# Kernel optimization log

Measured on AMD Instinct MI355X. Metric: run time of the kernel, lower is better.

## Reference

```python
import jax, jax.numpy as jnp
import numpy as np

B, S, D, H, F = 2, 2048, 1024, 16, 4096
DH = D // H


def setup_inputs() -> dict:
    key = jax.random.key(0)
    ks = jax.random.split(key, 8)
    scale = 0.02
    def nrm(k, shape):
        return jax.random.normal(k, shape, jnp.float32) * scale
    return {
        "x": jax.random.normal(ks[0], (B, S, D), jnp.float32),
        "ln1_g": jnp.ones((D,), jnp.float32),
        "ln1_b": jnp.zeros((D,), jnp.float32),
        "wq": nrm(ks[1], (D, D)), "bq": jnp.zeros((D,), jnp.float32),
        "wk": nrm(ks[2], (D, D)), "bk": jnp.zeros((D,), jnp.float32),
        "wv": nrm(ks[3], (D, D)), "bv": jnp.zeros((D,), jnp.float32),
        "wo": nrm(ks[4], (D, D)), "bo": jnp.zeros((D,), jnp.float32),
        "ln2_g": jnp.ones((D,), jnp.float32),
        "ln2_b": jnp.zeros((D,), jnp.float32),
        "w1": nrm(ks[5], (D, F)), "b1": jnp.zeros((F,), jnp.float32),
        "w2": nrm(ks[6], (F, D)), "b2": jnp.zeros((D,), jnp.float32),
    }


def _layernorm(x, g, b, eps=1e-5):
    m = jnp.mean(x, axis=-1, keepdims=True)
    v = jnp.var(x, axis=-1, keepdims=True)
    return (x - m) / jnp.sqrt(v + eps) * g + b


def reference(x, ln1_g, ln1_b, wq, bq, wk, bk, wv, bv, wo, bo,
              ln2_g, ln2_b, w1, b1, w2, b2):
    # GPT2Block forward, prefill path (state=None): K/V = ln_1(x), causal mask.
    Bx, Sx, Dx = x.shape
    h = _layernorm(x, ln1_g, ln1_b)

    def heads(t):  # [B,S,D] -> [B,H,S,DH]
        return t.reshape(Bx, Sx, H, DH).transpose(0, 2, 1, 3)

    q = heads(h @ wq + bq)
    k = heads(h @ wk + bk)
    v = heads(h @ wv + bv)

    scores = jnp.einsum('bhqd,bhkd->bhqk', q, k) / jnp.sqrt(jnp.float32(DH))
    # masked_softmax: key position < valid_len (= query_pos+1) kept; else -1e6
    causal = jnp.arange(Sx)[None, :] <= jnp.arange(Sx)[:, None]  # [S,S]
    scores = jnp.where(causal, scores, jnp.float32(-1e6))
    attn_w = jax.nn.softmax(scores, axis=-1)

    o = jnp.einsum('bhqk,bhkd->bhqd', attn_w, v)
    o = o.transpose(0, 2, 1, 3).reshape(Bx, Sx, Dx)
    attn_out = o @ wo + bo

    add1 = x + attn_out  # dropout inactive (eval)
    h2 = _layernorm(add1, ln2_g, ln2_b)
    mlp = jax.nn.gelu(h2 @ w1 + b1, approximate=False) @ w2 + b2
    return add1 + mlp
```

## Files before the change

### kernel.cpp

```cpp
#include <hip/hip_runtime.h>
#include <hip/hip_bf16.h>


#define BDIM 1024
#define SEQ 2048
#define NH 16
#define DHEAD 64
#define FDIM 4096
#define QKVD 3072

typedef __attribute__((ext_vector_type(8))) short short8v;
typedef __attribute__((ext_vector_type(4))) float floatx4;

__device__ __forceinline__ unsigned short f2bf(float f) {
    unsigned int u = __float_as_uint(f);
    unsigned int r = u + 0x7FFFu + ((u >> 16) & 1u);
    return (unsigned short)(r >> 16);
}
__device__ __forceinline__ unsigned int pack2bf(float a, float b) {
    return (unsigned int)f2bf(a) | ((unsigned int)f2bf(b) << 16);
}

__device__ __forceinline__ void load16_lds(const unsigned short* g, short* l) {
    __builtin_amdgcn_global_load_lds((const __attribute__((address_space(1))) void*)g,
                                     (__attribute__((address_space(3))) void*)l, 16, 0, 0);
}

__global__ __launch_bounds__(256) void transpose_all(const float* __restrict__ wq,
                                                     const float* __restrict__ wk,
                                                     const float* __restrict__ wv,
                                                     const float* __restrict__ wo,
                                                     const float* __restrict__ w1,
                                                     const float* __restrict__ w2,
                                                     unsigned short* __restrict__ qkvT,
                                                     unsigned short* __restrict__ woT,
                                                     unsigned short* __restrict__ w1T,
                                                     unsigned short* __restrict__ w2T) {
    const int g = blockIdx.x;
    const float* W;
    unsigned short* Wt;
    int K, N, tx, ty;
    if (g < 4096) {
        const int w = g >> 10, tile = g & 1023;
        tx = tile & 31; ty = tile >> 5; K = 1024; N = 1024;
        W = (w == 0) ? wq : (w == 1) ? wk : (w == 2) ? wv : wo;
        Wt = (w == 3) ? woT : qkvT + (size_t)w * 1024 * 1024;
    } else if (g < 8192) {
        const int tile = g - 4096;
        tx = tile & 127; ty = tile >> 7; K = 1024; N = 4096;
        W = w1; Wt = w1T;
    } else {
        const int tile = g - 8192;
        tx = tile & 31; ty = tile >> 5; K = 4096; N = 1024;
        W = w2; Wt = w2T;
    }
    __shared__ float tile[32][33];
    const int t = threadIdx.x;
    const int r = t >> 3, c4 = (t & 7) * 4;
    const int n0 = tx * 32, k0 = ty * 32;
    float4 p = *(const float4*)(W + (size_t)(k0 + r) * N + n0 + c4);
    tile[r][c4 + 0] = p.x;
    tile[r][c4 + 1] = p.y;
    tile[r][c4 + 2] = p.z;
    tile[r][c4 + 3] = p.w;
    __syncthreads();
    ushort4 ou;
    ou.x = f2bf(tile[c4 + 0][r]);
    ou.y = f2bf(tile[c4 + 1][r]);
    ou.z = f2bf(tile[c4 + 2][r]);
    ou.w = f2bf(tile[c4 + 3][r]);
    *(ushort4*)(Wt + (size_t)(n0 + r) * K + k0 + c4) = ou;
}

__global__ void concat_bias(const float* __restrict__ a, const float* __restrict__ b,
                            const float* __restrict__ c, float* __restrict__ out) {
    int i = blockIdx.x * 256 + threadIdx.x;
    out[i] = (i < 1024) ? a[i] : (i < 2048 ? b[i - 1024] : c[i - 2048]);
}

__global__ __launch_bounds__(256) void ln_kernel(const float* __restrict__ x,
                                                 const float* __restrict__ g,
                                                 const float* __restrict__ bb,
                                                 unsigned short* __restrict__ out) {
    const int row = blockIdx.x;
    const int t = threadIdx.x;
    const int c = t * 4;
    float4 p = *(const float4*)(x + (size_t)row * BDIM + c);
    float s = p.x + p.y + p.z + p.w;
    float sq = p.x * p.x + p.y * p.y + p.z * p.z + p.w * p.w;
    for (int off = 1; off < 64; off <<= 1) {
        s += __shfl_xor(s, off);
        sq += __shfl_xor(sq, off);
    }
    __shared__ float ssum[4], ssq[4];
    const int wave = t >> 6, lane = t & 63;
    if (lane == 0) { ssum[wave] = s; ssq[wave] = sq; }
    __syncthreads();
    s = ssum[0] + ssum[1] + ssum[2] + ssum[3];
    sq = ssq[0] + ssq[1] + ssq[2] + ssq[3];
    const float mean = s * (1.0f / BDIM);
    const float var = sq * (1.0f / BDIM) - mean * mean;
    const float rstd = rsqrtf(var + 1e-5f);
    float4 gg = *(const float4*)(g + c);
    float4 bv = *(const float4*)(bb + c);
    ushort4 o;
    o.x = f2bf((p.x - mean) * rstd * gg.x + bv.x);
    o.y = f2bf((p.y - mean) * rstd * gg.y + bv.y);
    o.z = f2bf((p.z - mean) * rstd * gg.z + bv.z);
    o.w = f2bf((p.w - mean) * rstd * gg.w + bv.w);
    *(ushort4*)(out + (size_t)row * BDIM + c) = o;
}

template <int BN, int RES, int GELU, int OBF16, int QSCALE = 0, int VOUT = 0>
__global__ __launch_bounds__(256, 3) void mfma_gemm(const unsigned short* __restrict__ A,
                                                    const unsigned short* __restrict__ Bt,
                                                    const float* __restrict__ bias,
                                                    const float* __restrict__ res,
                                                    void* __restrict__ Cv,
                                                    unsigned short* __restrict__ vtout,
                                                    int M, int N, int K) {
    constexpr int MI = (BN == 128) ? 4 : 2;
    __shared__ short As[2][128 * 32];
    __shared__ short Bs[2][BN * 32];
    const int t = threadIdx.x;
    const int wave = t >> 6, lane = t & 63;
    const int m0 = blockIdx.y * 128, n0 = blockIdx.x * BN;
    const int wmrow = (BN == 128) ? (wave & 1) * 64 : wave * 32;
    const int wnrow = (BN == 128) ? (wave >> 1) * 64 : 0;
    const int mlane = lane & 15, quad = lane >> 4;

    floatx4 acc[MI][4];
#pragma unroll
    for (int mi = 0; mi < MI; ++mi)
#pragma unroll
        for (int ni = 0; ni < 4; ++ni) {
            floatx4 z = {0.0f, 0.0f, 0.0f, 0.0f};
            acc[mi][ni] = z;
        }

    auto stage = [&](int buf, int k0) {
#pragma unroll
        for (int j = 0; j < 2; ++j) {
            const int c = j * 256 + t;
            load16_lds(A + (size_t)(m0 + (c >> 2)) * K + k0 + (c & 3) * 8, &As[buf][c * 8]);
        }
#pragma unroll
        for (int j = 0; j < BN / 64; ++j) {
            const int c = j * 256 + t;
            load16_lds(Bt + (size_t)(n0 + (c >> 2)) * K + k0 + (c & 3) * 8, &Bs[buf][c * 8]);
        }
    };

    stage(0, 0);
    const int nt = K >> 5;
#pragma unroll 2
    for (int i = 0; i < nt; ++i) {
        const int buf = i & 1;
        __syncthreads();
        if (i + 1 < nt) stage(buf ^ 1, (i + 1) << 5);
        short8v a[MI], b[4];
#pragma unroll
        for (int mi = 0; mi < MI; ++mi)
            a[mi] = *(const short8v*)&As[buf][(wmrow + mi * 16 + mlane) * 32 + quad * 8];
#pragma unroll
        for (int ni = 0; ni < 4; ++ni)
            b[ni] = *(const short8v*)&Bs[buf][(wnrow + ni * 16 + mlane) * 32 + quad * 8];
#pragma unroll
        for (int mi = 0; mi < MI; ++mi)
#pragma unroll
            for (int ni = 0; ni < 4; ++ni)
                acc[mi][ni] = __builtin_amdgcn_mfma_f32_16x16x32_bf16(b[ni], a[mi], acc[mi][ni], 0, 0, 0);
    }

#pragma unroll
    for (int mi = 0; mi < MI; ++mi) {
        const int row = m0 + wmrow + mi * 16 + mlane;
#pragma unroll
        for (int ni = 0; ni < 4; ++ni) {
            const int col0 = n0 + wnrow + ni * 16 + quad * 4;
            const float4 bv4 = *(const float4*)(bias + col0);
            float v0 = acc[mi][ni][0] + bv4.x;
            float v1 = acc[mi][ni][1] + bv4.y;
            float v2 = acc[mi][ni][2] + bv4.z;
            float v3 = acc[mi][ni][3] + bv4.w;
            if (VOUT && col0 >= 2048) {
                const int vd0 = col0 - 2048;
                const int bb = row >> 11, ss = row & 2047;
                unsigned short* vp =
                    vtout + ((size_t)(bb * NH + (vd0 >> 6)) * DHEAD + (vd0 & 63)) * SEQ + ss;
                vp[0 * SEQ] = f2bf(v0);
                vp[1 * SEQ] = f2bf(v1);
                vp[2 * SEQ] = f2bf(v2);
                vp[3 * SEQ] = f2bf(v3);
            } else {
                if (RES) {
                    const float4 r4 = *(const float4*)(res + (size_t)row * N + col0);
                    v0 += r4.x; v1 += r4.y; v2 += r4.z; v3 += r4.w;
                }
                if (GELU) {
                    v0 = 0.5f * v0 * (1.0f + erff(v0 * 0.70710678118654752f));
                    v1 = 0.5f * v1 * (1.0f + erff(v1 * 0.70710678118654752f));
                    v2 = 0.5f * v2 * (1.0f + erff(v2 * 0.70710678118654752f));
                    v3 = 0.5f * v3 * (1.0f + erff(v3 * 0.70710678118654752f));
                }
                if (QSCALE && col0 < 1024) {
                    v0 *= 0.18033688011112042f;
                    v1 *= 0.18033688011112042f;
                    v2 *= 0.18033688011112042f;
                    v3 *= 0.18033688011112042f;
                }
                if (OBF16) {
                    uint2 pk;
                    pk.x = pack2bf(v0, v1);
                    pk.y = pack2bf(v2, v3);
                    *(uint2*)((unsigned short*)Cv + (size_t)row * N + col0) = pk;
                } else {
                    float4 o4 = {v0, v1, v2, v3};
                    *(float4*)((float*)Cv + (size_t)row * N + col0) = o4;
                }
            }
        }
    }
}

__global__ __launch_bounds__(512, 4) void attn_kernel(const unsigned short* __restrict__ qkv,
                                                      const unsigned short* __restrict__ vt,
                                                      unsigned short* __restrict__ o) {
    const int g = blockIdx.x;
    const int qt = (g < 256) ? (15 - (g >> 5)) : ((g - 256) >> 5);
    const int hb = g & 31;
    const int h = hb & 15, b = hb >> 4;
    const int t = threadIdx.x;
    const int wave = t >> 6, lane = t & 63;
    const int mlane = lane & 15, quad = lane >> 4;
    const int msw = mlane & 7;
    const int wq0 = qt * 128 + wave * 16;
    const size_t bS = (size_t)b * SEQ;

    __shared__ unsigned short Ks[64][64];
    __shared__ unsigned short Vs[64][64];
    __shared__ __align__(16) unsigned short plds[8][16][64];

    short8v qf0, qf1;
    {
        const unsigned short* qrow = qkv + (bS + wq0 + mlane) * QKVD + h * DHEAD;
        qf0 = *(const short8v*)(qrow + quad * 8);
        qf1 = *(const short8v*)(qrow + 32 + quad * 8);
    }

    const unsigned short* kbase = qkv + bS * QKVD + 1024 + h * DHEAD;
    const unsigned short* vbase = vt + ((size_t)(b * NH + h)) * DHEAD * SEQ;

    const int sr = t >> 3, sc = t & 7;
    const int ssw = (sc ^ (sr & 7)) * 8;
    const unsigned short* kg = kbase + (size_t)sr * QKVD + sc * 8;
    const unsigned short* vg = vbase + (size_t)sr * SEQ + sc * 8;

    floatx4 ot[4];
#pragma unroll
    for (int mt = 0; mt < 4; ++mt) { floatx4 z = {0, 0, 0, 0}; ot[mt] = z; }
    float m_r = -INFINITY, l_r = 0.0f;

    const int kend = wq0 + 16;
    const int kmax = qt * 128 + 128;

    uint4 kr = *(const uint4*)kg;
    uint4 vr = *(const uint4*)vg;

    for (int k0 = 0; k0 < kmax; k0 += 64) {
        *(uint4*)&Ks[sr][ssw] = kr;
        *(uint4*)&Vs[sr][ssw] = vr;
        __syncthreads();
        if (k0 + 64 < kmax) {
            kr = *(const uint4*)(kg + (size_t)(k0 + 64) * QKVD);
            vr = *(const uint4*)(vg + (k0 + 64));
        }
        if (k0 < kend) {
            floatx4 st[4];
#pragma unroll
            for (int kt = 0; kt < 4; ++kt) {
                if (k0 + kt * 16 < kend) {
                    short8v kfa = *(const short8v*)&Ks[kt * 16 + mlane][(quad ^ msw) * 8];
                    short8v kfb = *(const short8v*)&Ks[kt * 16 + mlane][((quad + 4) ^ msw) * 8];
                    floatx4 z = {0, 0, 0, 0};
                    st[kt] = __builtin_amdgcn_mfma_f32_16x16x32_bf16(kfa, qf0, z, 0, 0, 0);
                    st[kt] = __builtin_amdgcn_mfma_f32_16x16x32_bf16(kfb, qf1, st[kt], 0, 0, 0);
                } else {
                    floatx4 mz = {-1e30f, -1e30f, -1e30f, -1e30f};
                    st[kt] = mz;
                }
            }
            if (k0 + 64 >= kend) {
#pragma unroll
                for (int kt = 0; kt < 4; ++kt)
#pragma unroll
                    for (int rg = 0; rg < 4; ++rg)
                        if (k0 + kt * 16 + quad * 4 + rg > wq0 + mlane)
                            st[kt][rg] = -1e30f;
            }
            float tm = st[0][0];
#pragma unroll
            for (int kt = 0; kt < 4; ++kt)
#pragma unroll
                for (int rg = 0; rg < 4; ++rg) tm = fmaxf(tm, st[kt][rg]);
            tm = fmaxf(tm, __shfl_xor(tm, 16));
            tm = fmaxf(tm, __shfl_xor(tm, 32));
            if (!__all(tm <= m_r + 8.0f)) {
                const float newm = fmaxf(m_r, tm);
                const float alpha = exp2f(m_r - newm);
                l_r *= alpha;
#pragma unroll
                for (int mt = 0; mt < 4; ++mt)
#pragma unroll
                    for (int rg = 0; rg < 4; ++rg) ot[mt][rg] *= alpha;
                m_r = newm;
            }
            float p[4][4], psum = 0.0f;
#pragma unroll
            for (int kt = 0; kt < 4; ++kt)
#pragma unroll
                for (int rg = 0; rg < 4; ++rg) {
                    p[kt][rg] = exp2f(st[kt][rg] - m_r);
                    psum += p[kt][rg];
                }
            psum += __shfl_xor(psum, 16);
            psum += __shfl_xor(psum, 32);
            l_r += psum;
            char* prow = (char*)&plds[wave][mlane][0];
#pragma unroll
            for (int kt = 0; kt < 4; ++kt) {
                uint2 pk;
                pk.x = pack2bf(p[kt][0], p[kt][1]);
                pk.y = pack2bf(p[kt][2], p[kt][3]);
                *(uint2*)(prow + ((kt * 32 + quad * 8) ^ (msw << 4))) = pk;
            }
#pragma unroll
            for (int kh = 0; kh < 2; ++kh) {
                if (k0 + kh * 32 < kend) {
                    short8v vf[4];
#pragma unroll
                    for (int mt = 0; mt < 4; ++mt)
                        vf[mt] = *(const short8v*)&Vs[mt * 16 + mlane][(((kh * 4 + quad) ^ msw)) * 8];
                    short8v pf = *(const short8v*)(prow + (((kh * 4 + quad) ^ msw) << 4));
#pragma unroll
                    for (int mt = 0; mt < 4; ++mt)
                        ot[mt] = __builtin_amdgcn_mfma_f32_16x16x32_bf16(vf[mt], pf, ot[mt], 0, 0, 0);
                }
            }
        }
        __syncthreads();
    }

    const float inv = 1.0f / l_r;
    unsigned short* orow = o + (bS + wq0 + mlane) * BDIM + h * DHEAD;
#pragma unroll
    for (int mt = 0; mt < 4; ++mt) {
        uint2 pk;
        pk.x = pack2bf(ot[mt][0] * inv, ot[mt][1] * inv);
        pk.y = pack2bf(ot[mt][2] * inv, ot[mt][3] * inv);
        *(uint2*)(orow + mt * 16 + quad * 4) = pk;
    }
}

extern "C" void kernel_launch(void* const* d_in, const int* in_sizes, int n_in,
                              void* d_out, int out_size, void* d_ws, size_t ws_size,
                              hipStream_t stream) {
    const int M = 2 * SEQ;

    const float* x = (const float*)d_in[0];
    const float* ln1_g = (const float*)d_in[1];
    const float* ln1_b = (const float*)d_in[2];
    const float* wq = (const float*)d_in[3];
    const float* bq = (const float*)d_in[4];
    const float* wk = (const float*)d_in[5];
    const float* bk = (const float*)d_in[6];
    const float* wv = (const float*)d_in[7];
    const float* bv = (const float*)d_in[8];
    const float* wo = (const float*)d_in[9];
    const float* bo = (const float*)d_in[10];
    const float* ln2_g = (const float*)d_in[11];
    const float* ln2_b = (const float*)d_in[12];
    const float* w1 = (const float*)d_in[13];
    const float* b1 = (const float*)d_in[14];
    const float* w2 = (const float*)d_in[15];
    const float* b2 = (const float*)d_in[16];

    char* wsb = (char*)d_ws;
    unsigned short* qkv = (unsigned short*)wsb;
    unsigned short* ffn = (unsigned short*)wsb;
    unsigned short* vt = (unsigned short*)(wsb + (24u << 20));
    unsigned short* hbuf = (unsigned short*)(wsb + (32u << 20));
    float* add1 = (float*)(wsb + (40u << 20));
    unsigned short* h2 = (unsigned short*)(wsb + (56u << 20));
    unsigned short* qkvT = (unsigned short*)(wsb + (64u << 20));
    unsigned short* woT = (unsigned short*)(wsb + (70u << 20));
    unsigned short* w1T = (unsigned short*)(wsb + (72u << 20));
    unsigned short* w2T = (unsigned short*)(wsb + (80u << 20));
    float* bqkv = (float*)(wsb + (88u << 20));

    transpose_all<<<12288, 256, 0, stream>>>(wq, wk, wv, wo, w1, w2, qkvT, woT, w1T, w2T);
    concat_bias<<<12, 256, 0, stream>>>(bq, bk, bv, bqkv);

    ln_kernel<<<M, 256, 0, stream>>>(x, ln1_g, ln1_b, hbuf);

    mfma_gemm<128, 0, 0, 1, 1, 1><<<dim3(QKVD / 128, M / 128), 256, 0, stream>>>(
        hbuf, qkvT, bqkv, nullptr, qkv, vt, M, QKVD, 1024);

    attn_kernel<<<512, 512, 0, stream>>>(qkv, vt, hbuf);

    mfma_gemm<64, 1, 0, 0><<<dim3(1024 / 64, M / 128), 256, 0, stream>>>(
        hbuf, woT, bo, x, add1, nullptr, M, 1024, 1024);

    ln_kernel<<<M, 256, 0, stream>>>(add1, ln2_g, ln2_b, h2);

    mfma_gemm<128, 0, 1, 1><<<dim3(FDIM / 128, M / 128), 256, 0, stream>>>(
        h2, w1T, b1, nullptr, ffn, nullptr, M, FDIM, 1024);

    mfma_gemm<64, 1, 0, 0><<<dim3(1024 / 64, M / 128), 256, 0, stream>>>(
        ffn, w2T, b2, add1, (float*)d_out, nullptr, M, 1024, FDIM);
}
```

Measured before the change: 375.4 us.

## Triple-buffer GEMM LDS staging with vmcnt waits and remap workgroup order

The MFMA GEMM moves from a double-buffered LDS pipeline with a full __syncthreads per k-step to a three-stage ring with prefetch distance two. Each iteration waits only until the oldest stage has landed (s_waitcnt vmcnt), then issues a raw s_barrier. Block IDs are also remapped in strides of eight so that concurrently scheduled workgroups share A/B tiles in cache. The extra buffer raises LDS use per block, which may reduce occupancy under launch_bounds(256,3). The raw barrier and vmcnt counting also need to be correct to avoid races.

```diff
diff --git a/kernel.cpp b/kernel.cpp
--- a/kernel.cpp
+++ b/kernel.cpp
@@ -24,6 +24,11 @@
 __device__ __forceinline__ void load16_lds(const unsigned short* g, short* l) {
     __builtin_amdgcn_global_load_lds((const __attribute__((address_space(1))) void*)g,
                                      (__attribute__((address_space(3))) void*)l, 16, 0, 0);
+}
+
+template <int N>
+__device__ __forceinline__ void wait_vmcnt() {
+    asm volatile("s_waitcnt vmcnt(%0)" ::"n"(N) : "memory");
 }
 
 __global__ __launch_bounds__(256) void transpose_all(const float* __restrict__ wq,
@@ -120,11 +125,18 @@
                                                     unsigned short* __restrict__ vtout,
                                                     int M, int N, int K) {
     constexpr int MI = (BN == 128) ? 4 : 2;
-    __shared__ short As[2][128 * 32];
-    __shared__ short Bs[2][BN * 32];
+    constexpr int LPT = 2 + BN / 64;
+    __shared__ short As[3][128 * 32];
+    __shared__ short Bs[3][BN * 32];
     const int t = threadIdx.x;
     const int wave = t >> 6, lane = t & 63;
-    const int m0 = blockIdx.y * 128, n0 = blockIdx.x * BN;
+
+    const int nwg = gridDim.x * gridDim.y;
+    int bid = blockIdx.y * gridDim.x + blockIdx.x;
+    bid = (bid & 7) * (nwg >> 3) + (bid >> 3);
+    const int bx = bid % gridDim.x, by = bid / gridDim.x;
+    const int m0 = by * 128, n0 = bx * BN;
+
     const int wmrow = (BN == 128) ? (wave & 1) * 64 : wave * 32;
     const int wnrow = (BN == 128) ? (wave >> 1) * 64 : 0;
     const int mlane = lane & 15, quad = lane >> 4;
@@ -138,26 +150,29 @@
             acc[mi][ni] = z;
         }
 
-    auto stage = [&](int buf, int k0) {
+    auto stage = [&](int b, int k0) {
 #pragma unroll
         for (int j = 0; j < 2; ++j) {
             const int c = j * 256 + t;
-            load16_lds(A + (size_t)(m0 + (c >> 2)) * K + k0 + (c & 3) * 8, &As[buf][c * 8]);
+            load16_lds(A + (size_t)(m0 + (c >> 2)) * K + k0 + (c & 3) * 8, &As[b][c * 8]);
         }
 #pragma unroll
         for (int j = 0; j < BN / 64; ++j) {
             const int c = j * 256 + t;
-            load16_lds(Bt + (size_t)(n0 + (c >> 2)) * K + k0 + (c & 3) * 8, &Bs[buf][c * 8]);
+            load16_lds(Bt + (size_t)(n0 + (c >> 2)) * K + k0 + (c & 3) * 8, &Bs[b][c * 8]);
         }
     };
 
+    const int nt = K >> 5;
     stage(0, 0);
-    const int nt = K >> 5;
-#pragma unroll 2
+    stage(1, 32);
+    int buf = 0, sbuf = 2;
     for (int i = 0; i < nt; ++i) {
-        const int buf = i & 1;
-        __syncthreads();
-        if (i + 1 < nt) stage(buf ^ 1, (i + 1) << 5);
+        if (i + 1 < nt) wait_vmcnt<LPT>();
+        else wait_vmcnt<0>();
+        __builtin_amdgcn_s_barrier();
+        __builtin_amdgcn_sched_barrier(0);
+        if (i + 2 < nt) stage(sbuf, (i + 2) << 5);
         short8v a[MI], b[4];
 #pragma unroll
         for (int mi = 0; mi < MI; ++mi)
@@ -170,6 +185,8 @@
 #pragma unroll
             for (int ni = 0; ni < 4; ++ni)
                 acc[mi][ni] = __builtin_amdgcn_mfma_f32_16x16x32_bf16(b[ni], a[mi], acc[mi][ni], 0, 0, 0);
+        buf = (buf == 2) ? 0 : buf + 1;
+        sbuf = (sbuf == 2) ? 0 : sbuf + 1;
     }
 
 #pragma unroll
```

After: 388.8 us. 1.04x slower.
